# Performance work log

Hardware: AMD Instinct MI355X
Metric: run time of the kernel (lower is better)

Reference implementation:

```python
import jax, jax.numpy as jnp
import numpy as np

B, N, C = 4, 4096, 384
D = H3 = W3 = 16          # input_size
WS = 8                    # window_size (divides 16 -> no padding)
NH = 6                    # num_heads
HD = C // NH              # head_dim = 64


def setup_inputs() -> dict:
    key = jax.random.key(0)
    ks = jax.random.split(key, 8)
    return {
        "x": jax.random.normal(ks[0], (B, N, C), jnp.float32),
        "qkv_w": jax.random.normal(ks[1], (C, 3 * C), jnp.float32) * 0.02,
        "qkv_b": jax.random.normal(ks[2], (3 * C,), jnp.float32) * 0.02,
        "proj_w": jax.random.normal(ks[3], (C, C), jnp.float32) * 0.02,
        "proj_b": jax.random.normal(ks[4], (C,), jnp.float32) * 0.02,
        "rel_pos_x": jax.random.normal(ks[5], (2 * WS - 1, HD), jnp.float32) * 0.02,
        "rel_pos_y": jax.random.normal(ks[6], (2 * WS - 1, HD), jnp.float32) * 0.02,
        "rel_pos_z": jax.random.normal(ks[7], (2 * WS - 1, HD), jnp.float32) * 0.02,
    }


def reference(x, qkv_w, qkv_b, proj_w, proj_b, rel_pos_x, rel_pos_y, rel_pos_z):
    nd = D // WS                      # windows per spatial dim = 2
    b_ = B * nd * nd * nd             # 32 windows
    T = WS * WS * WS                  # 512 tokens per window
    scale = HD ** -0.5

    # window partition: [B,N,C] -> [b_, T, C]
    x3 = x.reshape(B, nd, WS, nd, WS, nd, WS, C)
    x3 = x3.transpose(0, 1, 3, 5, 2, 4, 6, 7)
    xf = x3.reshape(b_, T, C)

    # qkv projection
    qkv = xf @ qkv_w + qkv_b                                  # [b_, T, 3C]
    qkv = qkv.reshape(b_, T, 3, NH, HD).transpose(2, 0, 3, 1, 4)
    q, k, v = qkv[0], qkv[1], qkv[2]                          # [b_, NH, T, HD]

    attn = jnp.einsum('bhqc,bhkc->bhqk', q * scale, k)        # [b_, NH, T, T]

    # decomposed 3D relative position bias (q_size == k_size == WS)
    coords = jnp.arange(WS)[:, None] - jnp.arange(WS)[None, :] + (WS - 1)
    Rx = rel_pos_x[coords]                                    # [WS, WS, HD]
    Ry = rel_pos_y[coords]
    Rz = rel_pos_z[coords]
    rq = q.reshape(b_ * NH, WS, WS, WS, HD)
    rel_x = jnp.einsum('bdhwc,dkc->bdhwk', rq, Rx)
    rel_y = jnp.einsum('bdhwc,hkc->bdhwk', rq, Ry)
    rel_z = jnp.einsum('bdhwc,wkc->bdhwk', rq, Rz)
    a = attn.reshape(b_ * NH, WS, WS, WS, WS, WS, WS)
    a = (a + rel_x[:, :, :, :, :, None, None]
           + rel_y[:, :, :, :, None, :, None]
           + rel_z[:, :, :, :, None, None, :])
    attn = a.reshape(b_, NH, T, T)

    attn = jax.nn.softmax(attn, axis=-1)
    out = jnp.einsum('bhqk,bhkc->bhqc', attn, v)              # [b_, NH, T, HD]
    out = out.transpose(0, 2, 1, 3).reshape(b_, T, C)
    out = out @ proj_w + proj_b

    # window unpartition: [b_, T, C] -> [B, N, C]
    o = out.reshape(B, nd, nd, nd, WS, WS, WS, C)
    o = o.transpose(0, 1, 4, 2, 5, 3, 6, 7).reshape(B, D, H3, W3, C)
    return o.reshape(B, N, C)
```

## Files before the change

### kernel.cpp

```cpp
#include <hip/hip_runtime.h>
#include <hip/hip_bf16.h>

typedef __bf16 bf16_t;
typedef __bf16 bf16x8 __attribute__((ext_vector_type(8)));
typedef __bf16 bf16x4 __attribute__((ext_vector_type(4)));
typedef float f32x4 __attribute__((ext_vector_type(4)));

#define MFMA16(a, b, c) __builtin_amdgcn_mfma_f32_16x16x32_bf16((a), (b), (c), 0, 0, 0)

__device__ __forceinline__ f32x4 v4zero() {
  f32x4 z = {0.f, 0.f, 0.f, 0.f};
  return z;
}

__device__ __forceinline__ int xrow_of(int m) {
  int win = m >> 9, t = m & 511;
  int b = win >> 3, d1 = (win >> 2) & 1, h1 = (win >> 1) & 1, w1 = win & 1;
  int d2 = t >> 6, h2 = (t >> 3) & 7, w2 = t & 7;
  return (b << 12) | ((d1 * 8 + d2) << 8) | ((h1 * 8 + h2) << 4) | (w1 * 8 + w2);
}

__global__ __launch_bounds__(256) void qkv_kernel(
    const float* __restrict__ x, const float* __restrict__ w,
    const float* __restrict__ bias, bf16_t* __restrict__ qg,
    bf16_t* __restrict__ kg, bf16_t* __restrict__ vtg) {
  __shared__ __align__(16) char smem[40960];
  bf16_t(*As)[128][40] = (bf16_t(*)[128][40])smem;
  bf16_t(*Bs)[128][40] = (bf16_t(*)[128][40])(smem + 20480);
  bf16_t(*Csh)[136] = (bf16_t(*)[136])smem;

  const int tid = threadIdx.x;
  const int lane = tid & 63, wv = tid >> 6;
  const int m0 = blockIdx.x * 128, n0 = blockIdx.y * 128;

  const int arow = tid >> 1, aseg = tid & 1;
  const float* asrc = x + (size_t)xrow_of(m0 + arow) * 384 + aseg * 16;
  const int bn = tid & 127, bks = (tid >> 7) * 16;
  const float* bsrc = w + (size_t)bks * 1152 + n0 + bn;

  const int wr = (wv >> 1) * 64, wc = (wv & 1) * 64;
  const int lr = lane & 15, lg = lane >> 4, lk = lg * 8;

  f32x4 acc[4][4];
#pragma unroll
  for (int fr = 0; fr < 4; ++fr)
#pragma unroll
    for (int fc = 0; fc < 4; ++fc) acc[fr][fc] = v4zero();

  f32x4 afr[4];
  float bfr[16];

#define LOAD_TILE(kt)                                              \
  {                                                                \
    _Pragma("unroll") for (int i = 0; i < 4; ++i)                  \
        afr[i] = *(const f32x4*)(asrc + (kt)*32 + i * 4);          \
    _Pragma("unroll") for (int i = 0; i < 16; ++i)                 \
        bfr[i] = bsrc[(size_t)((kt)*32 + i) * 1152];               \
  }

#define STAGE_TILE(buf)                                            \
  {                                                                \
    bf16x8 a0, a1, b0, b1;                                         \
    _Pragma("unroll") for (int i = 0; i < 4; ++i) {                \
      a0[i] = (bf16_t)afr[0][i];                                   \
      a0[4 + i] = (bf16_t)afr[1][i];                               \
      a1[i] = (bf16_t)afr[2][i];                                   \
      a1[4 + i] = (bf16_t)afr[3][i];                               \
    }                                                              \
    _Pragma("unroll") for (int i = 0; i < 8; ++i) {                \
      b0[i] = (bf16_t)bfr[i];                                      \
      b1[i] = (bf16_t)bfr[8 + i];                                  \
    }                                                              \
    *(bf16x8*)&As[buf][arow][aseg * 16] = a0;                      \
    *(bf16x8*)&As[buf][arow][aseg * 16 + 8] = a1;                  \
    *(bf16x8*)&Bs[buf][bn][bks] = b0;                              \
    *(bf16x8*)&Bs[buf][bn][bks + 8] = b1;                          \
  }

  LOAD_TILE(0);
  STAGE_TILE(0);
  LOAD_TILE(1);
  __syncthreads();

  for (int kt = 0; kt < 12; ++kt) {
    const int cur = kt & 1;
    bf16x8 af[4], bfv[4];
#pragma unroll
    for (int fr = 0; fr < 4; ++fr) af[fr] = *(const bf16x8*)&As[cur][wr + fr * 16 + lr][lk];
#pragma unroll
    for (int fc = 0; fc < 4; ++fc) bfv[fc] = *(const bf16x8*)&Bs[cur][wc + fc * 16 + lr][lk];
#pragma unroll
    for (int fr = 0; fr < 4; ++fr)
#pragma unroll
      for (int fc = 0; fc < 4; ++fc)
        acc[fr][fc] = MFMA16(af[fr], bfv[fc], acc[fr][fc]);
    if (kt < 11) {
      STAGE_TILE(cur ^ 1);
      if (kt < 10) LOAD_TILE(kt + 2);
    }
    __syncthreads();
  }
#undef LOAD_TILE
#undef STAGE_TILE

  const int type = n0 / 384;
  if (type == 2) {
#pragma unroll
    for (int fc = 0; fc < 4; ++fc) {
      const int col = n0 + wc + fc * 16 + lr;
      const float bc = bias[col];
      const int cc = col - 768, hh = cc >> 6, c = cc & 63;
#pragma unroll
      for (int fr = 0; fr < 4; ++fr) {
        const int m = m0 + wr + fr * 16 + lg * 4;
        const int win = m >> 9, t = m & 511;
        bf16x4 pk;
#pragma unroll
        for (int r = 0; r < 4; ++r) pk[r] = (bf16_t)(acc[fr][fc][r] + bc);
        *(bf16x4*)(vtg + ((size_t)(win * 6 + hh) * 64 + c) * 512 + t) = pk;
      }
    }
  } else {
#pragma unroll
    for (int fc = 0; fc < 4; ++fc) {
      const int col = n0 + wc + fc * 16 + lr;
      const float bc = bias[col];
#pragma unroll
      for (int fr = 0; fr < 4; ++fr)
#pragma unroll
        for (int r = 0; r < 4; ++r)
          Csh[wr + fr * 16 + lg * 4 + r][wc + fc * 16 + lr] = (bf16_t)(acc[fr][fc][r] + bc);
    }
    __syncthreads();
    const int mloc = tid >> 1, half = tid & 1;
    const int hh2 = ((n0 - type * 384) >> 6) + half;
    const int m = m0 + mloc, win = m >> 9, t = m & 511;
    bf16_t* dst = (type == 0 ? qg : kg) + ((size_t)(win * 6 + hh2) * 512 + t) * 64;
#pragma unroll
    for (int j = 0; j < 8; ++j)
      *(bf16x8*)(dst + j * 8) = *(const bf16x8*)&Csh[mloc][half * 64 + j * 8];
  }
}

__global__ __launch_bounds__(256) void attn_kernel(
    const bf16_t* __restrict__ qg, const bf16_t* __restrict__ kg,
    const bf16_t* __restrict__ vtg, const float* __restrict__ rpx,
    const float* __restrict__ rpy, const float* __restrict__ rpz,
    bf16_t* __restrict__ ao) {
  __shared__ __align__(16) char smem[32768];
  __shared__ __align__(16) float rxT[8][132];
  const int tid = threadIdx.x, lane = tid & 63, wv = tid >> 6;
  const int hh = blockIdx.x, win = blockIdx.y, qt = blockIdx.z;
  const int wh = win * 6 + hh;
  const bf16_t* Qb = qg + (size_t)wh * 32768 + (size_t)qt * 8192;
  const bf16_t* Kb = kg + (size_t)wh * 32768;
  const bf16_t* Vb = vtg + (size_t)wh * 32768;

  bf16_t(*Qsh)[68] = (bf16_t(*)[68])smem;
  bf16_t(*Rsh)[68] = (bf16_t(*)[68])(smem + 17408);
  float(*Gsh)[132] = (float(*)[132])smem;
  bf16_t(*Ksh)[64][64] = (bf16_t(*)[64][64])smem;
  bf16_t(*Vsh)[64][64] = (bf16_t(*)[64][64])(smem + 16384);

  for (int i = tid; i < 1024; i += 256) {
    int row = i >> 3, slot = i & 7;
    *(bf16x8*)&Qsh[row][slot * 8] = *(const bf16x8*)(Qb + row * 64 + slot * 8);
  }
  for (int i = tid; i < 360; i += 256) {
    int row = i >> 3, slot = i & 7;
    int axis = row / 15, j = row - axis * 15;
    const float* RP = (axis == 0) ? rpx : (axis == 1) ? rpy : rpz;
    f32x4 r0 = *(const f32x4*)(RP + j * 64 + slot * 8);
    f32x4 r1 = *(const f32x4*)(RP + j * 64 + slot * 8 + 4);
    bf16x8 p;
#pragma unroll
    for (int jj = 0; jj < 4; ++jj) {
      p[jj] = (bf16_t)r0[jj];
      p[4 + jj] = (bf16_t)r1[jj];
    }
    *(bf16x8*)&Rsh[row][slot * 8] = p;
  }
  bf16x8 kreg[2], vreg[2];
#pragma unroll
  for (int r = 0; r < 2; ++r) {
    int ci = r * 256 + tid, row = ci >> 3, slot = ci & 7;
    kreg[r] = *(const bf16x8*)(Kb + (size_t)row * 64 + slot * 8);
    vreg[r] = *(const bf16x8*)(Vb + (size_t)row * 512 + slot * 8);
  }
  __syncthreads();

  const int lr = lane & 15, lg = lane >> 4;
  const int qrow0 = qt * 128 + wv * 32;
  const int qrb = wv * 32 + lr;

  bf16x8 bq[2][2];
#pragma unroll
  for (int fq = 0; fq < 2; ++fq)
#pragma unroll
    for (int ks = 0; ks < 2; ++ks)
      bq[fq][ks] = *(const bf16x8*)&Qsh[wv * 32 + fq * 16 + lr][ks * 32 + lg * 8];

  bf16x8 br[3][2];
#pragma unroll
  for (int jt = 0; jt < 3; ++jt)
#pragma unroll
    for (int ks = 0; ks < 2; ++ks)
      br[jt][ks] = *(const bf16x8*)&Rsh[jt * 16 + lr][ks * 32 + lg * 8];

  f32x4 gacc[2][3];
#pragma unroll
  for (int fq = 0; fq < 2; ++fq)
#pragma unroll
    for (int jt = 0; jt < 3; ++jt) {
      f32x4 g = MFMA16(bq[fq][0], br[jt][0], v4zero());
      gacc[fq][jt] = MFMA16(bq[fq][1], br[jt][1], g);
    }
  __syncthreads();

#pragma unroll
  for (int fq = 0; fq < 2; ++fq)
#pragma unroll
    for (int jt = 0; jt < 3; ++jt)
#pragma unroll
      for (int r = 0; r < 4; ++r)
        Gsh[jt * 16 + lr][(wv * 2 + fq) * 16 + lg * 4 + r] = gacc[fq][jt][r];
  __syncthreads();

  f32x4 byz[2][4];
#pragma unroll
  for (int fq = 0; fq < 2; ++fq) {
    const int q_r = qrb + fq * 16;
    const int qh_ = (q_r >> 3) & 7, qw_ = q_r & 7, qd_ = qt * 2 + (q_r >> 6);
#pragma unroll
    for (int fk = 0; fk < 4; ++fk) {
      f32x4 v;
#pragma unroll
      for (int i = 0; i < 4; ++i) {
        int kkl = fk * 16 + lg * 4 + i;
        v[i] = Gsh[15 + qh_ - (kkl >> 3) + 7][q_r] + Gsh[30 + qw_ - (kkl & 7) + 7][q_r];
      }
      byz[fq][fk] = v;
    }
    if (lg == 0) {
#pragma unroll
      for (int kt = 0; kt < 8; ++kt) rxT[kt][q_r] = Gsh[qd_ - kt + 7][q_r];
    }
  }
  __syncthreads();

#pragma unroll
  for (int r = 0; r < 2; ++r) {
    int ci = r * 256 + tid, row = ci >> 3, slot = ci & 7;
    *(bf16x8*)&Ksh[0][row][(slot ^ (row & 7)) * 8] = kreg[r];
    *(bf16x8*)&Vsh[0][row][(slot ^ (row & 7)) * 8] = vreg[r];
    kreg[r] = *(const bf16x8*)(Kb + (size_t)(64 + row) * 64 + slot * 8);
    vreg[r] = *(const bf16x8*)(Vb + (size_t)row * 512 + 64 + slot * 8);
  }
  __syncthreads();

  float rsum[2] = {0.f, 0.f};
  f32x4 oacc[2][4];
#pragma unroll
  for (int fq = 0; fq < 2; ++fq)
#pragma unroll
    for (int fc = 0; fc < 4; ++fc) oacc[fq][fc] = v4zero();

  for (int kt = 0; kt < 8; ++kt) {
    const int cur = kt & 1;
    bf16x8 ak[4][2];
#pragma unroll
    for (int fk = 0; fk < 4; ++fk) {
      const int row = fk * 16 + lr;
#pragma unroll
      for (int ks = 0; ks < 2; ++ks)
        ak[fk][ks] = *(const bf16x8*)&Ksh[cur][row][((ks * 4 + lg) ^ (row & 7)) * 8];
    }

    f32x4 sb[2][4];
#pragma unroll
    for (int fq = 0; fq < 2; ++fq) {
      const float rx = rxT[kt][qrb + fq * 16];
#pragma unroll
      for (int fk = 0; fk < 4; ++fk) {
        f32x4 s = MFMA16(ak[fk][0], bq[fq][0], v4zero());
        s = MFMA16(ak[fk][1], bq[fq][1], s);
        sb[fq][fk] = s * 0.125f + rx + byz[fq][fk];
      }
    }

#pragma unroll
    for (int fq = 0; fq < 2; ++fq) {
      float rs = 0.f;
#pragma unroll
      for (int fk = 0; fk < 4; ++fk)
#pragma unroll
        for (int i = 0; i < 4; ++i) {
          float p = __expf(sb[fq][fk][i]);
          sb[fq][fk][i] = p;
          rs += p;
        }
      rsum[fq] += rs;
    }

    bf16x8 pa[2][2];
#pragma unroll
    for (int fq = 0; fq < 2; ++fq)
#pragma unroll
      for (int h = 0; h < 2; ++h) {
#pragma unroll
        for (int j = 0; j < 4; ++j) {
          pa[fq][h][j] = (bf16_t)sb[fq][2 * h][j];
          pa[fq][h][4 + j] = (bf16_t)sb[fq][2 * h + 1][j];
        }
      }

#pragma unroll
    for (int h = 0; h < 2; ++h)
#pragma unroll
      for (int fc2 = 0; fc2 < 4; ++fc2) {
        const int row = fc2 * 16 + lr;
        const int c0 = (((h * 4 + (lg >> 1)) ^ (row & 7)) * 8) + (lg & 1) * 4;
        const int c1 = (((h * 4 + 2 + (lg >> 1)) ^ (row & 7)) * 8) + (lg & 1) * 4;
        bf16x4 v0 = *(const bf16x4*)&Vsh[cur][row][c0];
        bf16x4 v1 = *(const bf16x4*)&Vsh[cur][row][c1];
        bf16x8 bv;
#pragma unroll
        for (int j = 0; j < 4; ++j) {
          bv[j] = v0[j];
          bv[4 + j] = v1[j];
        }
#pragma unroll
        for (int fq = 0; fq < 2; ++fq)
          oacc[fq][fc2] = MFMA16(pa[fq][h], bv, oacc[fq][fc2]);
      }

    if (kt < 7) {
#pragma unroll
      for (int r = 0; r < 2; ++r) {
        int ci = r * 256 + tid, row = ci >> 3, slot = ci & 7;
        *(bf16x8*)&Ksh[cur ^ 1][row][(slot ^ (row & 7)) * 8] = kreg[r];
        *(bf16x8*)&Vsh[cur ^ 1][row][(slot ^ (row & 7)) * 8] = vreg[r];
        if (kt < 6) {
          kreg[r] = *(const bf16x8*)(Kb + (size_t)((kt + 2) * 64 + row) * 64 + slot * 8);
          vreg[r] = *(const bf16x8*)(Vb + (size_t)row * 512 + (kt + 2) * 64 + slot * 8);
        }
      }
    }
    __syncthreads();
  }

#pragma unroll
  for (int fq = 0; fq < 2; ++fq) {
    rsum[fq] += __shfl_xor(rsum[fq], 16);
    rsum[fq] += __shfl_xor(rsum[fq], 32);
  }
  f32x4 linv[2];
#pragma unroll
  for (int fq = 0; fq < 2; ++fq)
#pragma unroll
    for (int i = 0; i < 4; ++i)
      linv[fq][i] = 1.0f / __shfl(rsum[fq], lg * 4 + i);

#pragma unroll
  for (int fq = 0; fq < 2; ++fq)
#pragma unroll
    for (int fc2 = 0; fc2 < 4; ++fc2) {
      size_t base = ((size_t)win * 512 + qrow0 + fq * 16 + lg * 4) * 384 + hh * 64 + fc2 * 16 + lr;
#pragma unroll
      for (int i = 0; i < 4; ++i)
        ao[base + (size_t)i * 384] = (bf16_t)(oacc[fq][fc2][i] * linv[fq][i]);
    }
}

__global__ __launch_bounds__(256) void proj_kernel(
    const bf16_t* __restrict__ ain, const float* __restrict__ w,
    const float* __restrict__ bias, float* __restrict__ out) {
  __shared__ __align__(16) bf16_t At[128][40];
  __shared__ __align__(16) bf16_t Bt[128][40];
  const int tid = threadIdx.x;
  const int lane = tid & 63, wv = tid >> 6;
  const int m0 = blockIdx.x * 128, n0 = blockIdx.y * 128;

  const int arow = tid >> 1, aseg = tid & 1;
  const bf16_t* asrc = ain + (size_t)(m0 + arow) * 384 + aseg * 16;
  const int bn = tid & 127, bks = (tid >> 7) * 16;

  const int wr = (wv >> 1) * 64, wc = (wv & 1) * 64;
  const int lr = lane & 15, lk = (lane >> 4) * 8;

  f32x4 acc[4][4];
#pragma unroll
  for (int fr = 0; fr < 4; ++fr)
#pragma unroll
    for (int fc = 0; fc < 4; ++fc) acc[fr][fc] = v4zero();

  for (int kt = 0; kt < 12; ++kt) {
    bf16x8 a0 = *(const bf16x8*)(asrc + kt * 32);
    bf16x8 a1 = *(const bf16x8*)(asrc + kt * 32 + 8);
    bf16x8 b0, b1;
#pragma unroll
    for (int i = 0; i < 8; ++i)
      b0[i] = (bf16_t)w[(size_t)(kt * 32 + bks + i) * 384 + n0 + bn];
#pragma unroll
    for (int i = 0; i < 8; ++i)
      b1[i] = (bf16_t)w[(size_t)(kt * 32 + bks + 8 + i) * 384 + n0 + bn];
    *(bf16x8*)&At[arow][aseg * 16] = a0;
    *(bf16x8*)&At[arow][aseg * 16 + 8] = a1;
    *(bf16x8*)&Bt[bn][bks] = b0;
    *(bf16x8*)&Bt[bn][bks + 8] = b1;
    __syncthreads();
    bf16x8 af[4], bfv[4];
#pragma unroll
    for (int fr = 0; fr < 4; ++fr) af[fr] = *(const bf16x8*)&At[wr + fr * 16 + lr][lk];
#pragma unroll
    for (int fc = 0; fc < 4; ++fc) bfv[fc] = *(const bf16x8*)&Bt[wc + fc * 16 + lr][lk];
#pragma unroll
    for (int fr = 0; fr < 4; ++fr)
#pragma unroll
      for (int fc = 0; fc < 4; ++fc)
        acc[fr][fc] = MFMA16(af[fr], bfv[fc], acc[fr][fc]);
    __syncthreads();
  }

#pragma unroll
  for (int fc = 0; fc < 4; ++fc) {
    const int col = n0 + wc + fc * 16 + lr;
    const float bc = bias[col];
#pragma unroll
    for (int fr = 0; fr < 4; ++fr) {
      const int m = m0 + wr + fr * 16 + (lane >> 4) * 4;
#pragma unroll
      for (int r = 0; r < 4; ++r)
        out[(size_t)xrow_of(m + r) * 384 + col] = acc[fr][fc][r] + bc;
    }
  }
}

extern "C" void kernel_launch(void* const* d_in, const int* in_sizes, int n_in,
                              void* d_out, int out_size, void* d_ws, size_t ws_size,
                              hipStream_t stream) {
  (void)in_sizes; (void)n_in; (void)out_size;
  const float* x = (const float*)d_in[0];
  const float* qkv_w = (const float*)d_in[1];
  const float* qkv_b = (const float*)d_in[2];
  const float* proj_w = (const float*)d_in[3];
  const float* proj_b = (const float*)d_in[4];
  const float* rpx = (const float*)d_in[5];
  const float* rpy = (const float*)d_in[6];
  const float* rpz = (const float*)d_in[7];
  float* out = (float*)d_out;

  const size_t NE = 6291456;
  if (ws_size < NE * 4 * sizeof(bf16_t)) return;
  bf16_t* qg = (bf16_t*)d_ws;
  bf16_t* kg = qg + NE;
  bf16_t* vtg = kg + NE;
  bf16_t* ao = vtg + NE;

  qkv_kernel<<<dim3(128, 9), 256, 0, stream>>>(x, qkv_w, qkv_b, qg, kg, vtg);
  attn_kernel<<<dim3(6, 32, 4), 256, 0, stream>>>(qg, kg, vtg, rpx, rpy, rpz, ao);
  proj_kernel<<<dim3(128, 3), 256, 0, stream>>>(ao, proj_w, proj_b, out);
}
```

Before: 92.65 us.

## Deepen qkv prefetch to two register stages and double-buffer proj GEMM

The qkv GEMM now holds two register stages of global loads, so each tile is fetched two iterations ahead of its use instead of one. The proj GEMM gets the same double-buffered shared memory plus register prefetch pattern, replacing its load, sync, compute, sync loop. The goal is to hide global memory latency behind MFMA work, at the cost of more registers, which may lower occupancy.

```diff
diff --git a/kernel.cpp b/kernel.cpp
--- a/kernel.cpp
+++ b/kernel.cpp
@@ -47,29 +47,29 @@
 #pragma unroll
     for (int fc = 0; fc < 4; ++fc) acc[fr][fc] = v4zero();
 
-  f32x4 afr[4];
-  float bfr[16];
-
-#define LOAD_TILE(kt)                                              \
+  f32x4 afr[2][4];
+  float bfr[2][16];
+
+#define LOAD_TILE(kt, s)                                           \
   {                                                                \
     _Pragma("unroll") for (int i = 0; i < 4; ++i)                  \
-        afr[i] = *(const f32x4*)(asrc + (kt)*32 + i * 4);          \
+        afr[s][i] = *(const f32x4*)(asrc + (kt)*32 + i * 4);       \
     _Pragma("unroll") for (int i = 0; i < 16; ++i)                 \
-        bfr[i] = bsrc[(size_t)((kt)*32 + i) * 1152];               \
-  }
-
-#define STAGE_TILE(buf)                                            \
+        bfr[s][i] = bsrc[(size_t)((kt)*32 + i) * 1152];            \
+  }
+
+#define STAGE_TILE(s, buf)                                         \
   {                                                                \
     bf16x8 a0, a1, b0, b1;                                         \
     _Pragma("unroll") for (int i = 0; i < 4; ++i) {                \
-      a0[i] = (bf16_t)afr[0][i];                                   \
-      a0[4 + i] = (bf16_t)afr[1][i];                               \
-      a1[i] = (bf16_t)afr[2][i];                                   \
-      a1[4 + i] = (bf16_t)afr[3][i];                               \
+      a0[i] = (bf16_t)afr[s][0][i];                                \
+      a0[4 + i] = (bf16_t)afr[s][1][i];                            \
+      a1[i] = (bf16_t)afr[s][2][i];                                \
+      a1[4 + i] = (bf16_t)afr[s][3][i];                            \
     }                                                              \
     _Pragma("unroll") for (int i = 0; i < 8; ++i) {                \
-      b0[i] = (bf16_t)bfr[i];                                      \
-      b1[i] = (bf16_t)bfr[8 + i];                                  \
+      b0[i] = (bf16_t)bfr[s][i];                                   \
+      b1[i] = (bf16_t)bfr[s][8 + i];                               \
     }                                                              \
     *(bf16x8*)&As[buf][arow][aseg * 16] = a0;                      \
     *(bf16x8*)&As[buf][arow][aseg * 16 + 8] = a1;                  \
@@ -77,9 +77,10 @@
     *(bf16x8*)&Bs[buf][bn][bks + 8] = b1;                          \
   }
 
-  LOAD_TILE(0);
-  STAGE_TILE(0);
-  LOAD_TILE(1);
+  LOAD_TILE(0, 0);
+  LOAD_TILE(1, 1);
+  STAGE_TILE(0, 0);
+  LOAD_TILE(2, 0);
   __syncthreads();
 
   for (int kt = 0; kt < 12; ++kt) {
@@ -95,8 +96,8 @@
       for (int fc = 0; fc < 4; ++fc)
         acc[fr][fc] = MFMA16(af[fr], bfv[fc], acc[fr][fc]);
     if (kt < 11) {
-      STAGE_TILE(cur ^ 1);
-      if (kt < 10) LOAD_TILE(kt + 2);
+      STAGE_TILE((kt + 1) & 1, cur ^ 1);
+      if (kt < 9) LOAD_TILE(kt + 3, (kt + 3) & 1);
     }
     __syncthreads();
   }
@@ -375,8 +376,10 @@
 __global__ __launch_bounds__(256) void proj_kernel(
     const bf16_t* __restrict__ ain, const float* __restrict__ w,
     const float* __restrict__ bias, float* __restrict__ out) {
-  __shared__ __align__(16) bf16_t At[128][40];
-  __shared__ __align__(16) bf16_t Bt[128][40];
+  __shared__ __align__(16) char smem[40960];
+  bf16_t(*As)[128][40] = (bf16_t(*)[128][40])smem;
+  bf16_t(*Bs)[128][40] = (bf16_t(*)[128][40])(smem + 20480);
+
   const int tid = threadIdx.x;
   const int lane = tid & 63, wv = tid >> 6;
   const int m0 = blockIdx.x * 128, n0 = blockIdx.y * 128;
@@ -384,6 +387,7 @@
   const int arow = tid >> 1, aseg = tid & 1;
   const bf16_t* asrc = ain + (size_t)(m0 + arow) * 384 + aseg * 16;
   const int bn = tid & 127, bks = (tid >> 7) * 16;
+  const float* bsrc = w + (size_t)bks * 384 + n0 + bn;
 
   const int wr = (wv >> 1) * 64, wc = (wv & 1) * 64;
   const int lr = lane & 15, lk = (lane >> 4) * 8;
@@ -394,33 +398,55 @@
 #pragma unroll
     for (int fc = 0; fc < 4; ++fc) acc[fr][fc] = v4zero();
 
+  bf16x8 a0r, a1r;
+  float bfr[16];
+
+#define PLOAD(kt)                                                  \
+  {                                                                \
+    a0r = *(const bf16x8*)(asrc + (kt)*32);                        \
+    a1r = *(const bf16x8*)(asrc + (kt)*32 + 8);                    \
+    _Pragma("unroll") for (int i = 0; i < 16; ++i)                 \
+        bfr[i] = bsrc[(size_t)((kt)*32 + i) * 384];                \
+  }
+
+#define PSTAGE(buf)                                                \
+  {                                                                \
+    bf16x8 b0, b1;                                                 \
+    _Pragma("unroll") for (int i = 0; i < 8; ++i) {                \
+      b0[i] = (bf16_t)bfr[i];                                      \
+      b1[i] = (bf16_t)bfr[8 + i];                                  \
+    }                                                              \
+    *(bf16x8*)&As[buf][arow][aseg * 16] = a0r;                     \
+    *(bf16x8*)&As[buf][arow][aseg * 16 + 8] = a1r;                 \
+    *(bf16x8*)&Bs[buf][bn][bks] = b0;                              \
+    *(bf16x8*)&Bs[buf][bn][bks + 8] = b1;                          \
+  }
+
+  PLOAD(0);
+  PSTAGE(0);
+  PLOAD(1);
+  __syncthreads();
+
   for (int kt = 0; kt < 12; ++kt) {
-    bf16x8 a0 = *(const bf16x8*)(asrc + kt * 32);
-    bf16x8 a1 = *(const bf16x8*)(asrc + kt * 32 + 8);
-    bf16x8 b0, b1;
-#pragma unroll
-    for (int i = 0; i < 8; ++i)
-      b0[i] = (bf16_t)w[(size_t)(kt * 32 + bks + i) * 384 + n0 + bn];
-#pragma unroll
-    for (int i = 0; i < 8; ++i)
-      b1[i] = (bf16_t)w[(size_t)(kt * 32 + bks + 8 + i) * 384 + n0 + bn];
-    *(bf16x8*)&At[arow][aseg * 16] = a0;
-    *(bf16x8*)&At[arow][aseg * 16 + 8] = a1;
-    *(bf16x8*)&Bt[bn][bks] = b0;
-    *(bf16x8*)&Bt[bn][bks + 8] = b1;
-    __syncthreads();
+    const int cur = kt & 1;
     bf16x8 af[4], bfv[4];
 #pragma unroll
-    for (int fr = 0; fr < 4; ++fr) af[fr] = *(const bf16x8*)&At[wr + fr * 16 + lr][lk];
-#pragma unroll
-    for (int fc = 0; fc < 4; ++fc) bfv[fc] = *(const bf16x8*)&Bt[wc + fc * 16 + lr][lk];
+    for (int fr = 0; fr < 4; ++fr) af[fr] = *(const bf16x8*)&As[cur][wr + fr * 16 + lr][lk];
+#pragma unroll
+    for (int fc = 0; fc < 4; ++fc) bfv[fc] = *(const bf16x8*)&Bs[cur][wc + fc * 16 + lr][lk];
 #pragma unroll
     for (int fr = 0; fr < 4; ++fr)
 #pragma unroll
       for (int fc = 0; fc < 4; ++fc)
         acc[fr][fc] = MFMA16(af[fr], bfv[fc], acc[fr][fc]);
+    if (kt < 11) {
+      PSTAGE(cur ^ 1);
+      if (kt < 10) PLOAD(kt + 2);
+    }
     __syncthreads();
   }
+#undef PLOAD
+#undef PSTAGE
 
 #pragma unroll
   for (int fc = 0; fc < 4; ++fc) {
```

Result: slower. 159.8 us (+72.5%).
